# Optimization experiments

Measured on AMD Instinct MI355X. Metric: run time of the kernel, lower is better.

## Reference

```python
import jax, jax.numpy as jnp
import numpy as np

N, E, IN_CH, HID, HEADS, OUT = 50000, 800000, 128, 64, 2, 64
NEG_SLOPE = 0.2

def setup_inputs() -> dict:
    key = jax.random.key(0)
    ks = jax.random.split(key, 10)
    return {
        "x": jax.random.normal(ks[0], (N, IN_CH), dtype=jnp.float32),
        "edge_index": jax.random.randint(ks[1], (2, E), 0, N, dtype=jnp.int32),
        "W1": jax.random.normal(ks[2], (HEADS * HID, IN_CH), dtype=jnp.float32) * 0.05,
        "att1_src": jax.random.normal(ks[3], (HEADS, HID), dtype=jnp.float32) * 0.05,
        "att1_dst": jax.random.normal(ks[4], (HEADS, HID), dtype=jnp.float32) * 0.05,
        "b1": jax.random.normal(ks[5], (HEADS * HID,), dtype=jnp.float32) * 0.05,
        "W2": jax.random.normal(ks[6], (OUT, HEADS * HID), dtype=jnp.float32) * 0.05,
        "att2_src": jax.random.normal(ks[7], (1, OUT), dtype=jnp.float32) * 0.05,
        "att2_dst": jax.random.normal(ks[8], (1, OUT), dtype=jnp.float32) * 0.05,
        "b2": jax.random.normal(ks[9], (OUT,), dtype=jnp.float32) * 0.05,
    }

def _gat_conv(x, src, dst, W, a_src, a_dst, b, heads, out_ch, concat, n):
    # linear transform -> [N, H, C]
    h = (x @ W.T).reshape(n, heads, out_ch)
    # per-node attention halves: [N, H]
    alpha_s = (h * a_src[None]).sum(-1)
    alpha_d = (h * a_dst[None]).sum(-1)
    # per-edge raw score (messages flow src -> dst): [E, H]
    e = jax.nn.leaky_relu(alpha_s[src] + alpha_d[dst], negative_slope=NEG_SLOPE)
    # scatter-softmax normalized over each destination neighborhood
    m = jax.ops.segment_max(e, dst, num_segments=n)
    ex = jnp.exp(e - m[dst])
    denom = jax.ops.segment_sum(ex, dst, num_segments=n)
    alpha = ex / (denom[dst] + 1e-16)
    # weighted scatter-add of source features: [N, H, C]
    out = jax.ops.segment_sum(h[src] * alpha[:, :, None], dst, num_segments=n)
    out = out.reshape(n, heads * out_ch) if concat else out.mean(axis=1)
    return out + b

def reference(x, edge_index, W1, att1_src, att1_dst, b1, W2, att2_src, att2_dst, b2):
    n = x.shape[0]
    # PyG GATConv adds self-loops by default
    loops = jnp.arange(n, dtype=edge_index.dtype)
    src = jnp.concatenate([edge_index[0], loops])
    dst = jnp.concatenate([edge_index[1], loops])
    # dropout layers inactive (eval mode)
    h = _gat_conv(x, src, dst, W1, att1_src, att1_dst, b1, HEADS, HID, True, n)
    h = jax.nn.elu(h)
    out = _gat_conv(h, src, dst, W2, att2_src, att2_dst, b2, 1, OUT, False, n)
    return out
```

## Files before the change

kernel.cpp:

```cpp
#include <hip/hip_runtime.h>
#include <hip/hip_bf16.h>
#include <math.h>

typedef __bf16 bf16x8 __attribute__((ext_vector_type(8)));
typedef float f32x4 __attribute__((ext_vector_type(4)));
typedef float f32x2 __attribute__((ext_vector_type(2)));

__device__ __forceinline__ float lrelu(float x) { return x > 0.f ? x : 0.2f * x; }
__device__ __forceinline__ unsigned short f2bf(float f) {
    unsigned u = __float_as_uint(f);
    return (unsigned short)((u + 0x7fffu + ((u >> 16) & 1u)) >> 16);
}
__device__ __forceinline__ float bf16lo(unsigned u) { return __uint_as_float(u << 16); }
__device__ __forceinline__ float bf16hi(unsigned u) { return __uint_as_float(u & 0xffff0000u); }
__device__ __forceinline__ unsigned pkbf(float a, float b) {
    return (unsigned)f2bf(a) | ((unsigned)f2bf(b) << 16);
}
__device__ __forceinline__ float wred_sum(float v) {
#pragma unroll
    for (int o = 32; o; o >>= 1) v += __shfl_xor(v, o);
    return v;
}

__global__ __launch_bounds__(256) void cast_w(const float* __restrict__ W1,
                                              const float* __restrict__ W2,
                                              unsigned short* __restrict__ w1b,
                                              unsigned short* __restrict__ w2b) {
    int i = blockIdx.x * 256 + threadIdx.x;
    const float* src;
    unsigned short* dst;
    size_t off;
    if (i < 2048)      { src = W1; dst = w1b; off = (size_t)i * 8; }
    else if (i < 3072) { src = W2; dst = w2b; off = (size_t)(i - 2048) * 8; }
    else return;
    float4 v0 = *(const float4*)(src + off);
    float4 v1 = *(const float4*)(src + off + 4);
    union { unsigned short u[8]; uint4 q; } o;
    o.u[0] = f2bf(v0.x); o.u[1] = f2bf(v0.y); o.u[2] = f2bf(v0.z); o.u[3] = f2bf(v0.w);
    o.u[4] = f2bf(v1.x); o.u[5] = f2bf(v1.y); o.u[6] = f2bf(v1.z); o.u[7] = f2bf(v1.w);
    *(uint4*)(dst + off) = o.q;
}

__global__ __launch_bounds__(256) void k1_hist(const int* __restrict__ ei, int E, int Et,
                                               int* __restrict__ g_hist, int NB) {
    __shared__ int hist[256];
    int tid = threadIdx.x, b = blockIdx.x;
    hist[tid] = 0;
    __syncthreads();
    int base = b * 4096;
#pragma unroll
    for (int k = 0; k < 16; ++k) {
        int e = base + k * 256 + tid;
        if (e < Et) {
            int d = (e < E) ? ei[E + e] : (e - E);
            atomicAdd(&hist[d >> 8], 1);
        }
    }
    __syncthreads();
    g_hist[tid * NB + b] = hist[tid];
}

__global__ __launch_bounds__(256) void scan_p1(const int* __restrict__ in,
                                               int* __restrict__ partial, int n) {
    __shared__ int ws[4];
    int tid = threadIdx.x, lane = tid & 63, w = tid >> 6;
    int idx = blockIdx.x * 256 + tid;
    int v = (idx < n) ? in[idx] : 0;
    int s = v;
#pragma unroll
    for (int o = 32; o; o >>= 1) s += __shfl_xor(s, o);
    if (lane == 0) ws[w] = s;
    __syncthreads();
    if (tid == 0) partial[blockIdx.x] = ws[0] + ws[1] + ws[2] + ws[3];
}

__global__ __launch_bounds__(256) void scan_p2(int* __restrict__ partial, int nb) {
    __shared__ int ws[4];
    __shared__ int s_carry;
    int tid = threadIdx.x, lane = tid & 63, w = tid >> 6;
    if (tid == 0) s_carry = 0;
    __syncthreads();
    for (int base = 0; base < nb; base += 256) {
        int idx = base + tid;
        int v = (idx < nb) ? partial[idx] : 0;
        int incl = v;
#pragma unroll
        for (int off = 1; off < 64; off <<= 1) {
            int t = __shfl_up(incl, off);
            if (lane >= off) incl += t;
        }
        if (lane == 63) ws[w] = incl;
        __syncthreads();
        int wpre = 0;
        for (int k = 0; k < w; ++k) wpre += ws[k];
        int carry = s_carry;
        if (idx < nb) partial[idx] = carry + wpre + incl - v;
        __syncthreads();
        if (tid == 255) s_carry = carry + wpre + incl;
        __syncthreads();
    }
}

__global__ __launch_bounds__(256) void scan_p3g(const int* __restrict__ in,
                                                const int* __restrict__ partial,
                                                int* __restrict__ out, int n) {
    __shared__ int ws[4];
    int tid = threadIdx.x, lane = tid & 63, w = tid >> 6;
    int idx = blockIdx.x * 256 + tid;
    int v = (idx < n) ? in[idx] : 0;
    int incl = v;
#pragma unroll
    for (int off = 1; off < 64; off <<= 1) {
        int t = __shfl_up(incl, off);
        if (lane >= off) incl += t;
    }
    if (lane == 63) ws[w] = incl;
    __syncthreads();
    int wpre = 0;
    for (int k = 0; k < w; ++k) wpre += ws[k];
    if (idx < n) out[idx] = partial[blockIdx.x] + wpre + incl - v;
    if (idx == n - 1) out[n] = partial[blockIdx.x] + wpre + incl;
}

__global__ __launch_bounds__(256) void k3_scatter(const int* __restrict__ ei, int E, int Et,
                                                  const int* __restrict__ g_scan,
                                                  uint2* __restrict__ tmp, int NB) {
    __shared__ int hist[256], lofs[256], lcnt[256], gbase[256];
    __shared__ int ws4[4];
    __shared__ uint2 stage[4096];
    int tid = threadIdx.x, b = blockIdx.x;
    int lane = tid & 63, w = tid >> 6;
    int base = b * 4096;
    int valid = min(4096, Et - base);
    uint2 ev[16];
    hist[tid] = 0;
    lcnt[tid] = 0;
    gbase[tid] = g_scan[tid * NB + b];
    __syncthreads();
#pragma unroll
    for (int k = 0; k < 16; ++k) {
        int e = base + k * 256 + tid;
        if (e < Et) {
            int s, d;
            if (e < E) { s = ei[e]; d = ei[E + e]; } else { s = d = e - E; }
            ev[k] = make_uint2((unsigned)d, (unsigned)s);
            atomicAdd(&hist[d >> 8], 1);
        }
    }
    __syncthreads();
    {
        int v = hist[tid];
        int incl = v;
#pragma unroll
        for (int off = 1; off < 64; off <<= 1) {
            int t = __shfl_up(incl, off);
            if (lane >= off) incl += t;
        }
        if (lane == 63) ws4[w] = incl;
        __syncthreads();
        int wpre = 0;
        for (int k = 0; k < w; ++k) wpre += ws4[k];
        lofs[tid] = wpre + incl - v;
    }
    __syncthreads();
#pragma unroll
    for (int k = 0; k < 16; ++k) {
        int e = base + k * 256 + tid;
        if (e < Et) {
            int dg = ev[k].x >> 8;
            int r = atomicAdd(&lcnt[dg], 1);
            stage[lofs[dg] + r] = ev[k];
        }
    }
    __syncthreads();
    for (int j = tid; j < valid; j += 256) {
        uint2 v = stage[j];
        int dg = v.x >> 8;
        tmp[gbase[dg] + (j - lofs[dg])] = v;
    }
}

__global__ __launch_bounds__(256) void csr_finalize(const uint2* __restrict__ tmp,
                                                    const int* __restrict__ g_scan,
                                                    int* __restrict__ srcs,
                                                    int* __restrict__ rowptr,
                                                    int N, int Et, int NB) {
    __shared__ int cnt[256], lofs[256], lcnt[256];
    __shared__ int ws4[4];
    int tid = threadIdx.x, g = blockIdx.x;
    int lane = tid & 63, w = tid >> 6;
    int start = g_scan[g * NB];
    int end = g_scan[(g + 1) * NB];
    cnt[tid] = 0;
    lcnt[tid] = 0;
    __syncthreads();
    for (int e = start + tid; e < end; e += 256)
        atomicAdd(&cnt[tmp[e].x & 255u], 1);
    __syncthreads();
    {
        int v = cnt[tid];
        int incl = v;
#pragma unroll
        for (int off = 1; off < 64; off <<= 1) {
            int t = __shfl_up(incl, off);
            if (lane >= off) incl += t;
        }
        if (lane == 63) ws4[w] = incl;
        __syncthreads();
        int wpre = 0;
        for (int k = 0; k < w; ++k) wpre += ws4[k];
        lofs[tid] = wpre + incl - v;
    }
    __syncthreads();
    int d = g * 256 + tid;
    if (d < N) rowptr[d] = start + lofs[tid];
    if (d == N - 1) rowptr[N] = Et;
    for (int e = start + tid; e < end; e += 256) {
        uint2 v = tmp[e];
        int sub = v.x & 255u;
        int pos = start + lofs[sub] + atomicAdd(&lcnt[sub], 1);
        srcs[pos] = (int)v.y;
    }
}

template<int M, int H, bool AF32>
__global__ __launch_bounds__(256) void gemm_mfma(const void* __restrict__ Av,
                                                 const unsigned short* __restrict__ Wb,
                                                 const float* __restrict__ att_s,
                                                 const float* __restrict__ att_d,
                                                 unsigned short* __restrict__ Cb,
                                                 float* __restrict__ as_,
                                                 float* __restrict__ ad_,
                                                 int N) {
    constexpr int CT = M / 16;
    int tid = threadIdx.x;
    int wid = tid >> 6, l = tid & 63;
    int l15 = l & 15, lhi = l >> 4;
    int rowbase = blockIdx.x * 64 + wid * 16;
    f32x4 acc[CT] = {};

    int rc = min(rowbase + l15, N - 1);
    const unsigned short* ap = (const unsigned short*)Av + (size_t)rc * 128 + lhi * 8;
    const float* apf = (const float*)Av + (size_t)rc * 128 + lhi * 8;
    const unsigned short* wp = Wb + (size_t)l15 * 128 + lhi * 8;

#pragma unroll
    for (int ks = 0; ks < 4; ++ks) {
        int k0 = ks * 32;
        bf16x8 a;
        if (AF32) {
            float4 u0 = *(const float4*)(apf + k0);
            float4 u1 = *(const float4*)(apf + k0 + 4);
            union { unsigned short s[8]; bf16x8 v; } cc;
            cc.s[0] = f2bf(u0.x); cc.s[1] = f2bf(u0.y); cc.s[2] = f2bf(u0.z); cc.s[3] = f2bf(u0.w);
            cc.s[4] = f2bf(u1.x); cc.s[5] = f2bf(u1.y); cc.s[6] = f2bf(u1.z); cc.s[7] = f2bf(u1.w);
            a = cc.v;
        } else {
            a = *reinterpret_cast<const bf16x8*>(ap + k0);
        }
#pragma unroll
        for (int ct = 0; ct < CT; ++ct) {
            bf16x8 b = *reinterpret_cast<const bf16x8*>(wp + (size_t)ct * 16 * 128 + k0);
            acc[ct] = __builtin_amdgcn_mfma_f32_16x16x32_bf16(a, b, acc[ct], 0, 0, 0);
        }
    }

    int rbase = rowbase + lhi * 4;
#pragma unroll
    for (int j = 0; j < 4; ++j) {
        int gr = rbase + j;
        if (gr < N) {
#pragma unroll
            for (int ct = 0; ct < CT; ++ct)
                Cb[(size_t)gr * M + ct * 16 + l15] = f2bf(acc[ct][j]);
        }
    }
#pragma unroll
    for (int hd = 0; hd < H; ++hd) {
        float ps0 = 0.f, ps1 = 0.f, ps2 = 0.f, ps3 = 0.f;
        float pd0 = 0.f, pd1 = 0.f, pd2 = 0.f, pd3 = 0.f;
#pragma unroll
        for (int c4 = 0; c4 < 4; ++c4) {
            int ct = hd * 4 + c4;
            float ws = att_s[hd * 64 + c4 * 16 + l15];
            float wd = att_d[hd * 64 + c4 * 16 + l15];
            ps0 += acc[ct][0] * ws; pd0 += acc[ct][0] * wd;
            ps1 += acc[ct][1] * ws; pd1 += acc[ct][1] * wd;
            ps2 += acc[ct][2] * ws; pd2 += acc[ct][2] * wd;
            ps3 += acc[ct][3] * ws; pd3 += acc[ct][3] * wd;
        }
#pragma unroll
        for (int o = 1; o < 16; o <<= 1) {
            ps0 += __shfl_xor(ps0, o); pd0 += __shfl_xor(pd0, o);
            ps1 += __shfl_xor(ps1, o); pd1 += __shfl_xor(pd1, o);
            ps2 += __shfl_xor(ps2, o); pd2 += __shfl_xor(pd2, o);
            ps3 += __shfl_xor(ps3, o); pd3 += __shfl_xor(pd3, o);
        }
        if (l15 == 0) {
            int gr = rbase;
            if (gr < N)     { as_[(size_t)gr * H + hd] = ps0; ad_[(size_t)gr * H + hd] = pd0; }
            if (gr + 1 < N) { as_[(size_t)(gr + 1) * H + hd] = ps1; ad_[(size_t)(gr + 1) * H + hd] = pd1; }
            if (gr + 2 < N) { as_[(size_t)(gr + 2) * H + hd] = ps2; ad_[(size_t)(gr + 2) * H + hd] = pd2; }
            if (gr + 3 < N) { as_[(size_t)(gr + 3) * H + hd] = ps3; ad_[(size_t)(gr + 3) * H + hd] = pd3; }
        }
    }
}

template<int H, bool DO_ELU>
__global__ __launch_bounds__(256) void gat_agg(const int* __restrict__ rowptr,
                                               const int* __restrict__ srcs,
                                               const float* __restrict__ as_,
                                               const float* __restrict__ ad_,
                                               const unsigned* __restrict__ hfeat,
                                               const float* __restrict__ bias,
                                               void* __restrict__ outp, int N) {
    constexpr int RW = 32 * H;
    constexpr int G  = (H == 2) ? 4 : 8;
    constexpr int GL = 64 / G;
    __shared__ uint4 sent[4][64];
    int wid = threadIdx.x >> 6, lane = threadIdx.x & 63;
    int il = lane & (GL - 1);
    int grp = lane >> ((H == 2) ? 4 : 3);
    int d = blockIdx.x * 4 + wid;
    if (d >= N) return;
    int r0 = rowptr[d], r1 = rowptr[d + 1];
    int cnt = r1 - r0;
    float uad[H];
    if (H == 2) {
        float2 adp = *(const float2*)(ad_ + 2 * (size_t)d);
        uad[0] = adp.x; uad[H - 1] = adp.y;
    } else {
        uad[0] = ad_[d];
    }
    f32x2 A01 = {0.f, 0.f}, A23 = {0.f, 0.f}, A45 = {0.f, 0.f}, A67 = {0.f, 0.f};
    const char* hflb = (const char*)hfeat + 16 * il;
    bool hhi = (H == 2) && (il >= 8);
    const unsigned* sbase = reinterpret_cast<const unsigned*>(&sent[wid][0]) + (hhi ? 2 : 0);

    if (cnt <= 64) {
        int i = r0 + lane;
        bool act = i < r1;
        int se = act ? srcs[i] : 0;
        float ax[H];
        if (H == 2) {
            float2 asp = *(const float2*)(as_ + 2 * (size_t)se);
            float ex0 = act ? __expf(lrelu(asp.x + uad[0])) : 0.f;
            float ex1 = act ? __expf(lrelu(asp.y + uad[1])) : 0.f;
            float den0 = wred_sum(ex0);
            float den1 = wred_sum(ex1);
            ax[0] = ex0 * __builtin_amdgcn_rcpf(den0 + 1e-16f);
            ax[H - 1] = ex1 * __builtin_amdgcn_rcpf(den1 + 1e-16f);
        } else {
            float ex = act ? __expf(lrelu(as_[se] + uad[0])) : 0.f;
            float den = wred_sum(ex);
            ax[0] = ex * __builtin_amdgcn_rcpf(den + 1e-16f);
        }
        unsigned off = (unsigned)(se * (RW * 4));
        sent[wid][lane] = make_uint4(off, __float_as_uint(ax[0]),
                                     off, __float_as_uint(ax[H - 1]));
        __threadfence_block();
#pragma unroll 2
        for (int t = 0; t < cnt; t += G) {
            uint2 en = *(const uint2*)(sbase + 4 * (t + grp));
            float af = __uint_as_float(en.y);
            uint4 u = *(const uint4*)(hflb + en.x);
            f32x2 c;
            c.x = bf16lo(u.x); c.y = bf16hi(u.x); A01 += af * c;
            c.x = bf16lo(u.y); c.y = bf16hi(u.y); A23 += af * c;
            c.x = bf16lo(u.z); c.y = bf16hi(u.z); A45 += af * c;
            c.x = bf16lo(u.w); c.y = bf16hi(u.w); A67 += af * c;
        }
    } else {
        float psum[H];
#pragma unroll
        for (int h = 0; h < H; ++h) psum[h] = 0.f;
        for (int base = r0; base < r1; base += 64) {
            int i = base + lane;
            bool act = i < r1;
            int s = act ? srcs[i] : 0;
#pragma unroll
            for (int h = 0; h < H; ++h) {
                float sc = lrelu(as_[(size_t)s * H + h] + uad[h]);
                psum[h] += act ? __expf(sc) : 0.f;
            }
        }
        float inv[H];
#pragma unroll
        for (int h = 0; h < H; ++h)
            inv[h] = __builtin_amdgcn_rcpf(wred_sum(psum[h]) + 1e-16f);
        for (int base = r0; base < r1; base += 64) {
            int i = base + lane;
            bool act = i < r1;
            int se = act ? srcs[i] : 0;
            float ax[H];
#pragma unroll
            for (int h = 0; h < H; ++h) {
                float sc = lrelu(as_[(size_t)se * H + h] + uad[h]);
                ax[h] = act ? __expf(sc) * inv[h] : 0.f;
            }
            int cntc = min(64, r1 - base);
            unsigned off = (unsigned)(se * (RW * 4));
            sent[wid][lane] = make_uint4(off, __float_as_uint(ax[0]),
                                         off, __float_as_uint(ax[H - 1]));
            __threadfence_block();
            for (int t = 0; t < cntc; t += G) {
                uint2 en = *(const uint2*)(sbase + 4 * (t + grp));
                float af = __uint_as_float(en.y);
                uint4 u = *(const uint4*)(hflb + en.x);
                f32x2 c;
                c.x = bf16lo(u.x); c.y = bf16hi(u.x); A01 += af * c;
                c.x = bf16lo(u.y); c.y = bf16hi(u.y); A23 += af * c;
                c.x = bf16lo(u.z); c.y = bf16hi(u.z); A45 += af * c;
                c.x = bf16lo(u.w); c.y = bf16hi(u.w); A67 += af * c;
            }
            __threadfence_block();
        }
    }

#pragma unroll
    for (int o = GL; o < 64; o <<= 1) {
        A01.x += __shfl_xor(A01.x, o); A01.y += __shfl_xor(A01.y, o);
        A23.x += __shfl_xor(A23.x, o); A23.y += __shfl_xor(A23.y, o);
        A45.x += __shfl_xor(A45.x, o); A45.y += __shfl_xor(A45.y, o);
        A67.x += __shfl_xor(A67.x, o); A67.y += __shfl_xor(A67.y, o);
    }
    if (grp == 0) {
        int c0 = 8 * il;
        float4 bA = *(const float4*)(bias + c0);
        float4 bB = *(const float4*)(bias + c0 + 4);
        float v0 = A01.x + bA.x, v1 = A01.y + bA.y, v2 = A23.x + bA.z, v3 = A23.y + bA.w;
        float v4 = A45.x + bB.x, v5 = A45.y + bB.y, v6 = A67.x + bB.z, v7 = A67.y + bB.w;
        if (DO_ELU) {
            v0 = v0 > 0.f ? v0 : expm1f(v0); v1 = v1 > 0.f ? v1 : expm1f(v1);
            v2 = v2 > 0.f ? v2 : expm1f(v2); v3 = v3 > 0.f ? v3 : expm1f(v3);
            v4 = v4 > 0.f ? v4 : expm1f(v4); v5 = v5 > 0.f ? v5 : expm1f(v5);
            v6 = v6 > 0.f ? v6 : expm1f(v6); v7 = v7 > 0.f ? v7 : expm1f(v7);
        }
        if (H == 2) {
            uint4 o;
            o.x = pkbf(v0, v1); o.y = pkbf(v2, v3);
            o.z = pkbf(v4, v5); o.w = pkbf(v6, v7);
            *(uint4*)((unsigned*)outp + (size_t)d * 64 + 4 * il) = o;
        } else {
            *(float4*)((float*)outp + (size_t)d * 64 + c0) = make_float4(v0, v1, v2, v3);
            *(float4*)((float*)outp + (size_t)d * 64 + c0 + 4) = make_float4(v4, v5, v6, v7);
        }
    }
}

extern "C" void kernel_launch(void* const* d_in, const int* in_sizes, int n_in,
                              void* d_out, int out_size, void* d_ws, size_t ws_size,
                              hipStream_t stream) {
    const float* x   = (const float*)d_in[0];
    const int*   ei  = (const int*)d_in[1];
    const float* W1  = (const float*)d_in[2];
    const float* a1s = (const float*)d_in[3];
    const float* a1d = (const float*)d_in[4];
    const float* b1  = (const float*)d_in[5];
    const float* W2  = (const float*)d_in[6];
    const float* a2s = (const float*)d_in[7];
    const float* a2d = (const float*)d_in[8];
    const float* b2  = (const float*)d_in[9];
    float* out = (float*)d_out;

    int N  = in_sizes[0] / 128;
    int E  = in_sizes[1] / 2;
    int Et = E + N;
    int NB = (Et + 4095) / 4096;
    int nh = 256 * NB;

    char* p = (char*)d_ws;
    unsigned short* h1b = (unsigned short*)p;   p += (size_t)N * 128 * 2;
    unsigned short* act1b = (unsigned short*)p; p += (size_t)N * 128 * 2;
    unsigned short* h2b = (unsigned short*)p;   p += (size_t)N * 64 * 2;
    unsigned short* w1b = (unsigned short*)p;   p += 128 * 128 * 2;
    unsigned short* w2b = (unsigned short*)p;   p += 64 * 128 * 2;
    uint2* tmp = (uint2*)p;                p += (size_t)Et * 8;
    int* g_hist = (int*)p;                 p += (size_t)nh * 4;
    int* g_scan = (int*)p;                 p += (size_t)(nh + 1) * 4;
    int* partial = (int*)p;                p += (size_t)((nh + 255) / 256) * 4;
    float* as1 = (float*)p;                p += (size_t)N * 2 * 4;
    float* ad1 = (float*)p;                p += (size_t)N * 2 * 4;
    float* as2 = (float*)p;                p += (size_t)N * 4;
    float* ad2 = (float*)p;                p += (size_t)N * 4;
    int* rowptr = (int*)p;                 p += (size_t)(N + 1) * 4;
    int* srcs = (int*)p;                   p += (size_t)Et * 4;

    int nbs = (nh + 255) / 256;
    k1_hist<<<NB, 256, 0, stream>>>(ei, E, Et, g_hist, NB);
    scan_p1<<<nbs, 256, 0, stream>>>(g_hist, partial, nh);
    scan_p2<<<1, 256, 0, stream>>>(partial, nbs);
    scan_p3g<<<nbs, 256, 0, stream>>>(g_hist, partial, g_scan, nh);
    k3_scatter<<<NB, 256, 0, stream>>>(ei, E, Et, g_scan, tmp, NB);
    csr_finalize<<<256, 256, 0, stream>>>(tmp, g_scan, srcs, rowptr, N, Et, NB);

    cast_w<<<12, 256, 0, stream>>>(W1, W2, w1b, w2b);

    gemm_mfma<128, 2, true><<<(N + 63) / 64, 256, 0, stream>>>(x, w1b, a1s, a1d, h1b, as1, ad1, N);
    gat_agg<2, true><<<(N + 3) / 4, 256, 0, stream>>>(rowptr, srcs, as1, ad1,
                                                      (const unsigned*)h1b, b1, act1b, N);

    gemm_mfma<64, 1, false><<<(N + 63) / 64, 256, 0, stream>>>(act1b, w2b, a2s, a2d, h2b, as2, ad2, N);
    gat_agg<1, false><<<(N + 3) / 4, 256, 0, stream>>>(rowptr, srcs, as2, ad2,
                                                       (const unsigned*)h2b, b2, out, N);
}
```

Before: 143.6 us.

## Fuse weight cast and layer-1 GEMM into CSR build kernels, pack edges to 32 bits

Weight casting now runs as extra blocks of the histogram kernel, and the first-layer GEMM with its attention dot products runs as extra blocks of the scatter kernel. This removes two launches and lets the GEMM overlap with the CSR build. Edges are packed into one 32-bit word (destination high 16 bits, source low 16 bits), which halves the temporary buffer traffic, and csr_finalize stages the source indices in LDS before writing them out coalesced. The packing assumes node ids fit in 16 bits (N=50000), so larger graphs would silently corrupt the edges. The bigger shared-memory footprint may also reduce occupancy.

```diff
diff --git a/kernel.cpp b/kernel.cpp
--- a/kernel.cpp
+++ b/kernel.cpp
@@ -22,29 +22,31 @@
     return v;
 }
 
-__global__ __launch_bounds__(256) void cast_w(const float* __restrict__ W1,
-                                              const float* __restrict__ W2,
-                                              unsigned short* __restrict__ w1b,
-                                              unsigned short* __restrict__ w2b) {
-    int i = blockIdx.x * 256 + threadIdx.x;
-    const float* src;
-    unsigned short* dst;
-    size_t off;
-    if (i < 2048)      { src = W1; dst = w1b; off = (size_t)i * 8; }
-    else if (i < 3072) { src = W2; dst = w2b; off = (size_t)(i - 2048) * 8; }
-    else return;
-    float4 v0 = *(const float4*)(src + off);
-    float4 v1 = *(const float4*)(src + off + 4);
-    union { unsigned short u[8]; uint4 q; } o;
-    o.u[0] = f2bf(v0.x); o.u[1] = f2bf(v0.y); o.u[2] = f2bf(v0.z); o.u[3] = f2bf(v0.w);
-    o.u[4] = f2bf(v1.x); o.u[5] = f2bf(v1.y); o.u[6] = f2bf(v1.z); o.u[7] = f2bf(v1.w);
-    *(uint4*)(dst + off) = o.q;
-}
 
 __global__ __launch_bounds__(256) void k1_hist(const int* __restrict__ ei, int E, int Et,
-                                               int* __restrict__ g_hist, int NB) {
+                                               int* __restrict__ g_hist, int NB,
+                                               const float* __restrict__ W1,
+                                               const float* __restrict__ W2,
+                                               unsigned short* __restrict__ w1b,
+                                               unsigned short* __restrict__ w2b) {
+    int tid = threadIdx.x, b = blockIdx.x;
+    if (b >= NB) {
+        int i = (b - NB) * 256 + tid;
+        const float* src;
+        unsigned short* dst;
+        size_t off;
+        if (i < 2048)      { src = W1; dst = w1b; off = (size_t)i * 8; }
+        else if (i < 3072) { src = W2; dst = w2b; off = (size_t)(i - 2048) * 8; }
+        else return;
+        float4 v0 = *(const float4*)(src + off);
+        float4 v1 = *(const float4*)(src + off + 4);
+        union { unsigned short u[8]; uint4 q; } o;
+        o.u[0] = f2bf(v0.x); o.u[1] = f2bf(v0.y); o.u[2] = f2bf(v0.z); o.u[3] = f2bf(v0.w);
+        o.u[4] = f2bf(v1.x); o.u[5] = f2bf(v1.y); o.u[6] = f2bf(v1.z); o.u[7] = f2bf(v1.w);
+        *(uint4*)(dst + off) = o.q;
+        return;
+    }
     __shared__ int hist[256];
-    int tid = threadIdx.x, b = blockIdx.x;
     hist[tid] = 0;
     __syncthreads();
     int base = b * 4096;
@@ -122,17 +124,91 @@
     if (idx == n - 1) out[n] = partial[blockIdx.x] + wpre + incl;
 }
 
-__global__ __launch_bounds__(256) void k3_scatter(const int* __restrict__ ei, int E, int Et,
-                                                  const int* __restrict__ g_scan,
-                                                  uint2* __restrict__ tmp, int NB) {
+__global__ __launch_bounds__(256) void k3_gemm1(const int* __restrict__ ei, int E, int Et,
+                                                const int* __restrict__ g_scan,
+                                                unsigned* __restrict__ tmp, int NB,
+                                                const float* __restrict__ x,
+                                                const unsigned short* __restrict__ Wb,
+                                                const float* __restrict__ att_s,
+                                                const float* __restrict__ att_d,
+                                                unsigned short* __restrict__ Cb,
+                                                float* __restrict__ as_,
+                                                float* __restrict__ ad_,
+                                                int N) {
+    int tid = threadIdx.x;
+    if (blockIdx.x >= NB) {
+        constexpr int CT = 8;
+        int wid = tid >> 6, l = tid & 63;
+        int l15 = l & 15, lhi = l >> 4;
+        int rowbase = (blockIdx.x - NB) * 64 + wid * 16;
+        f32x4 acc[CT] = {};
+        int rc = min(rowbase + l15, N - 1);
+        const float* apf = x + (size_t)rc * 128 + lhi * 8;
+        const unsigned short* wp = Wb + (size_t)l15 * 128 + lhi * 8;
+#pragma unroll
+        for (int ks = 0; ks < 4; ++ks) {
+            int k0 = ks * 32;
+            float4 u0 = *(const float4*)(apf + k0);
+            float4 u1 = *(const float4*)(apf + k0 + 4);
+            union { unsigned short s[8]; bf16x8 v; } cc;
+            cc.s[0] = f2bf(u0.x); cc.s[1] = f2bf(u0.y); cc.s[2] = f2bf(u0.z); cc.s[3] = f2bf(u0.w);
+            cc.s[4] = f2bf(u1.x); cc.s[5] = f2bf(u1.y); cc.s[6] = f2bf(u1.z); cc.s[7] = f2bf(u1.w);
+            bf16x8 a = cc.v;
+#pragma unroll
+            for (int ct = 0; ct < CT; ++ct) {
+                bf16x8 b = *reinterpret_cast<const bf16x8*>(wp + (size_t)ct * 16 * 128 + k0);
+                acc[ct] = __builtin_amdgcn_mfma_f32_16x16x32_bf16(a, b, acc[ct], 0, 0, 0);
+            }
+        }
+        int rbase = rowbase + lhi * 4;
+#pragma unroll
+        for (int j = 0; j < 4; ++j) {
+            int gr = rbase + j;
+            if (gr < N) {
+#pragma unroll
+                for (int ct = 0; ct < CT; ++ct)
+                    Cb[(size_t)gr * 128 + ct * 16 + l15] = f2bf(acc[ct][j]);
+            }
+        }
+#pragma unroll
+        for (int hd = 0; hd < 2; ++hd) {
+            float ps0 = 0.f, ps1 = 0.f, ps2 = 0.f, ps3 = 0.f;
+            float pd0 = 0.f, pd1 = 0.f, pd2 = 0.f, pd3 = 0.f;
+#pragma unroll
+            for (int c4 = 0; c4 < 4; ++c4) {
+                int ct = hd * 4 + c4;
+                float ws = att_s[hd * 64 + c4 * 16 + l15];
+                float wd = att_d[hd * 64 + c4 * 16 + l15];
+                ps0 += acc[ct][0] * ws; pd0 += acc[ct][0] * wd;
+                ps1 += acc[ct][1] * ws; pd1 += acc[ct][1] * wd;
+                ps2 += acc[ct][2] * ws; pd2 += acc[ct][2] * wd;
+                ps3 += acc[ct][3] * ws; pd3 += acc[ct][3] * wd;
+            }
+#pragma unroll
+            for (int o = 1; o < 16; o <<= 1) {
+                ps0 += __shfl_xor(ps0, o); pd0 += __shfl_xor(pd0, o);
+                ps1 += __shfl_xor(ps1, o); pd1 += __shfl_xor(pd1, o);
+                ps2 += __shfl_xor(ps2, o); pd2 += __shfl_xor(pd2, o);
+                ps3 += __shfl_xor(ps3, o); pd3 += __shfl_xor(pd3, o);
+            }
+            if (l15 == 0) {
+                int gr = rbase;
+                if (gr < N)     { as_[(size_t)gr * 2 + hd] = ps0; ad_[(size_t)gr * 2 + hd] = pd0; }
+                if (gr + 1 < N) { as_[(size_t)(gr + 1) * 2 + hd] = ps1; ad_[(size_t)(gr + 1) * 2 + hd] = pd1; }
+                if (gr + 2 < N) { as_[(size_t)(gr + 2) * 2 + hd] = ps2; ad_[(size_t)(gr + 2) * 2 + hd] = pd2; }
+                if (gr + 3 < N) { as_[(size_t)(gr + 3) * 2 + hd] = ps3; ad_[(size_t)(gr + 3) * 2 + hd] = pd3; }
+            }
+        }
+        return;
+    }
     __shared__ int hist[256], lofs[256], lcnt[256], gbase[256];
     __shared__ int ws4[4];
-    __shared__ uint2 stage[4096];
-    int tid = threadIdx.x, b = blockIdx.x;
+    __shared__ unsigned stage[4096];
+    int b = blockIdx.x;
     int lane = tid & 63, w = tid >> 6;
     int base = b * 4096;
     int valid = min(4096, Et - base);
-    uint2 ev[16];
+    unsigned pv[16];
     hist[tid] = 0;
     lcnt[tid] = 0;
     gbase[tid] = g_scan[tid * NB + b];
@@ -143,7 +219,7 @@
         if (e < Et) {
             int s, d;
             if (e < E) { s = ei[e]; d = ei[E + e]; } else { s = d = e - E; }
-            ev[k] = make_uint2((unsigned)d, (unsigned)s);
+            pv[k] = ((unsigned)d << 16) | (unsigned)s;
             atomicAdd(&hist[d >> 8], 1);
         }
     }
@@ -167,35 +243,37 @@
     for (int k = 0; k < 16; ++k) {
         int e = base + k * 256 + tid;
         if (e < Et) {
-            int dg = ev[k].x >> 8;
+            int dg = pv[k] >> 24;
             int r = atomicAdd(&lcnt[dg], 1);
-            stage[lofs[dg] + r] = ev[k];
+            stage[lofs[dg] + r] = pv[k];
         }
     }
     __syncthreads();
     for (int j = tid; j < valid; j += 256) {
-        uint2 v = stage[j];
-        int dg = v.x >> 8;
+        unsigned v = stage[j];
+        int dg = v >> 24;
         tmp[gbase[dg] + (j - lofs[dg])] = v;
     }
 }
 
-__global__ __launch_bounds__(256) void csr_finalize(const uint2* __restrict__ tmp,
+__global__ __launch_bounds__(256) void csr_finalize(const unsigned* __restrict__ tmp,
                                                     const int* __restrict__ g_scan,
                                                     int* __restrict__ srcs,
                                                     int* __restrict__ rowptr,
                                                     int N, int Et, int NB) {
     __shared__ int cnt[256], lofs[256], lcnt[256];
     __shared__ int ws4[4];
+    __shared__ unsigned short sstage[8192];
     int tid = threadIdx.x, g = blockIdx.x;
     int lane = tid & 63, w = tid >> 6;
     int start = g_scan[g * NB];
     int end = g_scan[(g + 1) * NB];
+    int sz = end - start;
     cnt[tid] = 0;
     lcnt[tid] = 0;
     __syncthreads();
     for (int e = start + tid; e < end; e += 256)
-        atomicAdd(&cnt[tmp[e].x & 255u], 1);
+        atomicAdd(&cnt[(tmp[e] >> 16) & 255u], 1);
     __syncthreads();
     {
         int v = cnt[tid];
@@ -215,16 +293,28 @@
     int d = g * 256 + tid;
     if (d < N) rowptr[d] = start + lofs[tid];
     if (d == N - 1) rowptr[N] = Et;
-    for (int e = start + tid; e < end; e += 256) {
-        uint2 v = tmp[e];
-        int sub = v.x & 255u;
-        int pos = start + lofs[sub] + atomicAdd(&lcnt[sub], 1);
-        srcs[pos] = (int)v.y;
-    }
-}
-
-template<int M, int H, bool AF32>
-__global__ __launch_bounds__(256) void gemm_mfma(const void* __restrict__ Av,
+    if (sz <= 8192) {
+        for (int e = start + tid; e < end; e += 256) {
+            unsigned v = tmp[e];
+            int sub = (v >> 16) & 255u;
+            int pos = lofs[sub] + atomicAdd(&lcnt[sub], 1);
+            sstage[pos] = (unsigned short)(v & 0xffffu);
+        }
+        __syncthreads();
+        for (int j = tid; j < sz; j += 256)
+            srcs[start + j] = (int)sstage[j];
+    } else {
+        for (int e = start + tid; e < end; e += 256) {
+            unsigned v = tmp[e];
+            int sub = (v >> 16) & 255u;
+            int pos = start + lofs[sub] + atomicAdd(&lcnt[sub], 1);
+            srcs[pos] = (int)(v & 0xffffu);
+        }
+    }
+}
+
+template<int M, int H>
+__global__ __launch_bounds__(256) void gemm_mfma(const unsigned short* __restrict__ Ab,
                                                  const unsigned short* __restrict__ Wb,
                                                  const float* __restrict__ att_s,
                                                  const float* __restrict__ att_d,
@@ -240,24 +330,13 @@
     f32x4 acc[CT] = {};
 
     int rc = min(rowbase + l15, N - 1);
-    const unsigned short* ap = (const unsigned short*)Av + (size_t)rc * 128 + lhi * 8;
-    const float* apf = (const float*)Av + (size_t)rc * 128 + lhi * 8;
+    const unsigned short* ap = Ab + (size_t)rc * 128 + lhi * 8;
     const unsigned short* wp = Wb + (size_t)l15 * 128 + lhi * 8;
 
 #pragma unroll
     for (int ks = 0; ks < 4; ++ks) {
         int k0 = ks * 32;
-        bf16x8 a;
-        if (AF32) {
-            float4 u0 = *(const float4*)(apf + k0);
-            float4 u1 = *(const float4*)(apf + k0 + 4);
-            union { unsigned short s[8]; bf16x8 v; } cc;
-            cc.s[0] = f2bf(u0.x); cc.s[1] = f2bf(u0.y); cc.s[2] = f2bf(u0.z); cc.s[3] = f2bf(u0.w);
-            cc.s[4] = f2bf(u1.x); cc.s[5] = f2bf(u1.y); cc.s[6] = f2bf(u1.z); cc.s[7] = f2bf(u1.w);
-            a = cc.v;
-        } else {
-            a = *reinterpret_cast<const bf16x8*>(ap + k0);
-        }
+        bf16x8 a = *reinterpret_cast<const bf16x8*>(ap + k0);
 #pragma unroll
         for (int ct = 0; ct < CT; ++ct) {
             bf16x8 b = *reinterpret_cast<const bf16x8*>(wp + (size_t)ct * 16 * 128 + k0);
@@ -475,7 +554,7 @@
     unsigned short* h2b = (unsigned short*)p;   p += (size_t)N * 64 * 2;
     unsigned short* w1b = (unsigned short*)p;   p += 128 * 128 * 2;
     unsigned short* w2b = (unsigned short*)p;   p += 64 * 128 * 2;
-    uint2* tmp = (uint2*)p;                p += (size_t)Et * 8;
+    unsigned* tmp = (unsigned*)p;          p += (size_t)Et * 4;
     int* g_hist = (int*)p;                 p += (size_t)nh * 4;
     int* g_scan = (int*)p;                 p += (size_t)(nh + 1) * 4;
     int* partial = (int*)p;                p += (size_t)((nh + 255) / 256) * 4;
@@ -487,20 +566,19 @@
     int* srcs = (int*)p;                   p += (size_t)Et * 4;
 
     int nbs = (nh + 255) / 256;
-    k1_hist<<<NB, 256, 0, stream>>>(ei, E, Et, g_hist, NB);
+    int gemm1_blocks = (N + 63) / 64;
+    k1_hist<<<NB + 12, 256, 0, stream>>>(ei, E, Et, g_hist, NB, W1, W2, w1b, w2b);
     scan_p1<<<nbs, 256, 0, stream>>>(g_hist, partial, nh);
     scan_p2<<<1, 256, 0, stream>>>(partial, nbs);
     scan_p3g<<<nbs, 256, 0, stream>>>(g_hist, partial, g_scan, nh);
-    k3_scatter<<<NB, 256, 0, stream>>>(ei, E, Et, g_scan, tmp, NB);
+    k3_gemm1<<<NB + gemm1_blocks, 256, 0, stream>>>(ei, E, Et, g_scan, tmp, NB,
+                                                    x, w1b, a1s, a1d, h1b, as1, ad1, N);
     csr_finalize<<<256, 256, 0, stream>>>(tmp, g_scan, srcs, rowptr, N, Et, NB);
 
-    cast_w<<<12, 256, 0, stream>>>(W1, W2, w1b, w2b);
-
-    gemm_mfma<128, 2, true><<<(N + 63) / 64, 256, 0, stream>>>(x, w1b, a1s, a1d, h1b, as1, ad1, N);
     gat_agg<2, true><<<(N + 3) / 4, 256, 0, stream>>>(rowptr, srcs, as1, ad1,
                                                       (const unsigned*)h1b, b1, act1b, N);
 
-    gemm_mfma<64, 1, false><<<(N + 63) / 64, 256, 0, stream>>>(act1b, w2b, a2s, a2d, h2b, as2, ad2, N);
+    gemm_mfma<64, 1><<<(N + 63) / 64, 256, 0, stream>>>(act1b, w2b, a2s, a2d, h2b, as2, ad2, N);
     gat_agg<1, false><<<(N + 3) / 4, 256, 0, stream>>>(rowptr, srcs, as2, ad2,
                                                        (const unsigned*)h2b, b2, out, N);
 }
```

New measurement: 127.1 us, median of 2. 1.13x faster.
